# Kernel optimization log

Hardware: AMD Instinct MI355X
Metric: run time of the kernel (lower is better)

## Reference

```python
import jax, jax.numpy as jnp
import numpy as np

N_FILLERS = 10000
N_ROLES = 256
FILLER_DIM = 256
ROLE_DIM = 256
HIDDEN = 1024
B, S = 64, 128


def setup_inputs() -> dict:
    key = jax.random.key(0)
    k1, k2, k3, k4, k5, k6 = jax.random.split(key, 6)
    roles = jax.random.randint(k1, (B, S), 0, N_ROLES, dtype=jnp.int64 if jax.config.jax_enable_x64 else jnp.int32)
    hidden = jax.random.normal(k2, (1, B, HIDDEN), dtype=jnp.float32)
    filler_emb = jax.random.normal(k3, (N_FILLERS, FILLER_DIM), dtype=jnp.float32)
    role_emb = jax.random.normal(k4, (N_ROLES, ROLE_DIM), dtype=jnp.float32)
    role_emb = role_emb.at[0].set(0.0)  # padding_idx=0
    W = jax.random.normal(k5, (FILLER_DIM * ROLE_DIM, HIDDEN), dtype=jnp.float32) / np.sqrt(HIDDEN)
    b = jax.random.normal(k6, (FILLER_DIM * ROLE_DIM,), dtype=jnp.float32) * 0.01
    return {"roles": roles, "hidden": hidden, "filler_emb": filler_emb, "role_emb": role_emb, "W": W, "b": b}


def reference(roles, hidden, filler_emb, role_emb, W, b):
    fd = filler_emb.shape[1]
    rd = role_emb.shape[1]
    # input_layer: (1, B, hidden) -> (1, B, fd*rd)
    h = hidden @ W.T + b
    # transpose(0,1).transpose(1,2).view(-1, fd, rd): (B, fd, rd)
    h = jnp.transpose(h, (1, 2, 0)).reshape(-1, fd, rd)
    # role embedding with padding_idx=0 (row 0 is zero)
    role_table = role_emb.at[0].set(0.0)
    roles_e = role_table[roles]  # (B, S, rd)
    # bmm(roles_emb, hidden^T): (B, S, rd) x (B, rd, fd) -> (B, S, fd)
    fg = jnp.einsum('bsr,bfr->bsf', roles_e, h)
    # L2 distance to filler codebook via squared-norm trick: (B, S, n_fillers)
    d2 = (jnp.sum(fg * fg, axis=-1, keepdims=True)
          - 2.0 * jnp.einsum('bsf,nf->bsn', fg, filler_emb)
          + jnp.sum(filler_emb * filler_emb, axis=-1))
    dists = jnp.sqrt(jnp.maximum(d2, 0.0))
    log_probs = jax.nn.log_softmax(-dists, axis=-1)  # (B, S, n_fillers)
    preds = jnp.argmax(log_probs, axis=-1)  # top-1 indices, (B, S)
    return log_probs, preds
```

## Files before the change

### kernel.cpp

```cpp
#include <hip/hip_runtime.h>
#include <hip/hip_bf16.h>
#include <float.h>
#include <math.h>

#define ROWS 8192
#define NF   10000
#define NPAD 10240

typedef short s8v __attribute__((ext_vector_type(8)));
typedef float f4v __attribute__((ext_vector_type(4)));

#define GLD16(g, l) __builtin_amdgcn_global_load_lds((const __attribute__((address_space(1))) void*)(g), (__attribute__((address_space(3))) void*)(l), 16, 0, 0)

__device__ inline unsigned short f2bf(float x) {
  __hip_bfloat16 h = __float2bfloat16(x);
  return __builtin_bit_cast(unsigned short, h);
}
__device__ inline float bf2f(unsigned short u) {
  __hip_bfloat16 h = __builtin_bit_cast(__hip_bfloat16, u);
  return __bfloat162float(h);
}

__global__ __launch_bounds__(256) void k_cvt_filler(const float* __restrict__ filler,
                                                    unsigned short* __restrict__ fl2,
                                                    float* __restrict__ fln) {
  int row = blockIdx.x * 4 + (threadIdx.x >> 6);
  int lane = threadIdx.x & 63;
  if (row >= NPAD) return;
  if (row < NF) {
    float4 v = reinterpret_cast<const float4*>(filler + (size_t)row * 256)[lane];
    float s = v.x * v.x + v.y * v.y + v.z * v.z + v.w * v.w;
    #pragma unroll
    for (int off = 32; off >= 1; off >>= 1) s += __shfl_xor(s, off, 64);
    if (lane == 0) fln[row] = s;
    float xs[4] = {v.x, v.y, v.z, v.w};
    unsigned short h[4], lo[4];
    #pragma unroll
    for (int j = 0; j < 4; ++j) { h[j] = f2bf(xs[j]); lo[j] = f2bf(xs[j] - bf2f(h[j])); }
    uint2 hh = make_uint2(h[0] | ((unsigned)h[1] << 16), h[2] | ((unsigned)h[3] << 16));
    uint2 ll = make_uint2(lo[0] | ((unsigned)lo[1] << 16), lo[2] | ((unsigned)lo[3] << 16));
    *reinterpret_cast<uint2*>(fl2 + (size_t)row * 512 + lane * 4) = hh;
    *reinterpret_cast<uint2*>(fl2 + (size_t)row * 512 + 256 + lane * 4) = ll;
  } else {
    *reinterpret_cast<uint2*>(fl2 + (size_t)row * 512 + lane * 4) = make_uint2(0, 0);
    *reinterpret_cast<uint2*>(fl2 + (size_t)row * 512 + 256 + lane * 4) = make_uint2(0, 0);
    if (lane == 0) fln[row] = 1e30f;
  }
}

__global__ __launch_bounds__(256) void k_gemm1(const float* __restrict__ hidden,
                                               const float* __restrict__ W,
                                               const float* __restrict__ bias,
                                               float* __restrict__ ht) {
  __shared__ float As[64][68];
  __shared__ float Bs[64][136];
  __shared__ float biasS[128];
  const int tid = threadIdx.x;
  const int nbase = blockIdx.x * 128;
  const int r = nbase >> 8;
  const int f0 = nbase & 255;
  const int tm = tid >> 4, tn = tid & 15;
  const int m0 = tm * 4, n0 = tn * 8;

  if (tid < 128) biasS[tid] = bias[(size_t)(f0 + tid) * 256 + r];

  float acc[4][8];
  #pragma unroll
  for (int i = 0; i < 4; ++i)
    #pragma unroll
    for (int j = 0; j < 8; ++j) acc[i][j] = 0.f;

  for (int kt = 0; kt < 16; ++kt) {
    __syncthreads();
    #pragma unroll
    for (int i = 0; i < 4; ++i) {
      int q = tid + i * 256;
      int b = q >> 4, kq = q & 15;
      float4 v = *reinterpret_cast<const float4*>(hidden + (size_t)b * 1024 + kt * 64 + kq * 4);
      As[kq * 4 + 0][b] = v.x;
      As[kq * 4 + 1][b] = v.y;
      As[kq * 4 + 2][b] = v.z;
      As[kq * 4 + 3][b] = v.w;
    }
    #pragma unroll
    for (int i = 0; i < 8; ++i) {
      int q = tid + i * 256;
      int nl = q >> 4, kq = q & 15;
      size_t wrow = (size_t)(f0 + nl) * 256 + r;
      float4 v = *reinterpret_cast<const float4*>(W + wrow * 1024 + kt * 64 + kq * 4);
      Bs[kq * 4 + 0][nl] = v.x;
      Bs[kq * 4 + 1][nl] = v.y;
      Bs[kq * 4 + 2][nl] = v.z;
      Bs[kq * 4 + 3][nl] = v.w;
    }
    __syncthreads();
    #pragma unroll
    for (int kk = 0; kk < 64; ++kk) {
      float4 a  = *reinterpret_cast<const float4*>(&As[kk][m0]);
      float4 b0 = *reinterpret_cast<const float4*>(&Bs[kk][n0]);
      float4 b1 = *reinterpret_cast<const float4*>(&Bs[kk][n0 + 4]);
      float av[4] = {a.x, a.y, a.z, a.w};
      float bv[8] = {b0.x, b0.y, b0.z, b0.w, b1.x, b1.y, b1.z, b1.w};
      #pragma unroll
      for (int i = 0; i < 4; ++i)
        #pragma unroll
        for (int j = 0; j < 8; ++j) acc[i][j] += av[i] * bv[j];
    }
  }
  #pragma unroll
  for (int i = 0; i < 4; ++i) {
    int b = m0 + i;
    float4 o0 = make_float4(acc[i][0] + biasS[n0 + 0], acc[i][1] + biasS[n0 + 1],
                            acc[i][2] + biasS[n0 + 2], acc[i][3] + biasS[n0 + 3]);
    float4 o1 = make_float4(acc[i][4] + biasS[n0 + 4], acc[i][5] + biasS[n0 + 5],
                            acc[i][6] + biasS[n0 + 6], acc[i][7] + biasS[n0 + 7]);
    float* p = ht + (size_t)b * 65536 + nbase + n0;
    *reinterpret_cast<float4*>(p)     = o0;
    *reinterpret_cast<float4*>(p + 4) = o1;
  }
}

__global__ __launch_bounds__(256) void k_fg2(const int* __restrict__ roles,
                                             const float* __restrict__ role_emb,
                                             const float* __restrict__ ht,
                                             unsigned short* __restrict__ fg2,
                                             float* __restrict__ fgn) {
  __shared__ float As[64][40];
  __shared__ float Bs[64][264];
  __shared__ int sidx[32];
  const int tid = threadIdx.x;
  const int b = blockIdx.x >> 2;
  const int sbase = (blockIdx.x & 3) * 32;
  const int tm = tid >> 5, tn = tid & 31;
  const int m0 = tm * 4, n0 = tn * 8;
  if (tid < 32) sidx[tid] = roles[b * 128 + sbase + tid];

  float acc[4][8];
  #pragma unroll
  for (int i = 0; i < 4; ++i)
    #pragma unroll
    for (int j = 0; j < 8; ++j) acc[i][j] = 0.f;

  for (int kt = 0; kt < 4; ++kt) {
    __syncthreads();
    #pragma unroll
    for (int i = 0; i < 2; ++i) {
      int q = tid + i * 256;
      int s = q >> 4, rq = q & 15;
      float4 v = *reinterpret_cast<const float4*>(role_emb + (size_t)sidx[s] * 256 + kt * 64 + rq * 4);
      As[rq * 4 + 0][s] = v.x;
      As[rq * 4 + 1][s] = v.y;
      As[rq * 4 + 2][s] = v.z;
      As[rq * 4 + 3][s] = v.w;
    }
    #pragma unroll
    for (int i = 0; i < 16; ++i) {
      int q = tid + i * 256;
      int rr = q >> 6, fq = q & 63;
      float4 v = *reinterpret_cast<const float4*>(ht + (size_t)b * 65536 + (size_t)(kt * 64 + rr) * 256 + fq * 4);
      *reinterpret_cast<float4*>(&Bs[rr][fq * 4]) = v;
    }
    __syncthreads();
    #pragma unroll
    for (int kk = 0; kk < 64; ++kk) {
      float4 a  = *reinterpret_cast<const float4*>(&As[kk][m0]);
      float4 b0 = *reinterpret_cast<const float4*>(&Bs[kk][n0]);
      float4 b1 = *reinterpret_cast<const float4*>(&Bs[kk][n0 + 4]);
      float av[4] = {a.x, a.y, a.z, a.w};
      float bv[8] = {b0.x, b0.y, b0.z, b0.w, b1.x, b1.y, b1.z, b1.w};
      #pragma unroll
      for (int i = 0; i < 4; ++i)
        #pragma unroll
        for (int j = 0; j < 8; ++j) acc[i][j] += av[i] * bv[j];
    }
  }
  #pragma unroll
  for (int i = 0; i < 4; ++i) {
    const int grow = b * 128 + sbase + m0 + i;
    float nrm = 0.f;
    unsigned int hp[4], lp[4];
    #pragma unroll
    for (int j = 0; j < 8; j += 2) {
      float x0 = acc[i][j], x1 = acc[i][j + 1];
      nrm += x0 * x0 + x1 * x1;
      unsigned short h0 = f2bf(x0), h1 = f2bf(x1);
      unsigned short l0 = f2bf(x0 - bf2f(h0)), l1 = f2bf(x1 - bf2f(h1));
      hp[j >> 1] = h0 | ((unsigned)h1 << 16);
      lp[j >> 1] = l0 | ((unsigned)l1 << 16);
    }
    *reinterpret_cast<uint4*>(fg2 + (size_t)grow * 512 + n0)       = make_uint4(hp[0], hp[1], hp[2], hp[3]);
    *reinterpret_cast<uint4*>(fg2 + (size_t)grow * 512 + 256 + n0) = make_uint4(lp[0], lp[1], lp[2], lp[3]);
    #pragma unroll
    for (int msk = 1; msk <= 16; msk <<= 1) nrm += __shfl_xor(nrm, msk, 64);
    if (tn == 0) fgn[grow] = nrm;
  }
}

__global__ __launch_bounds__(256, 2) void k_dist(const unsigned short* __restrict__ fg2,
                                                 const unsigned short* __restrict__ fl2,
                                                 const float* __restrict__ fgn,
                                                 const float* __restrict__ fln,
                                                 float* __restrict__ out) {
  __shared__ __align__(16) char lds[2][32768];
  __shared__ float rn2s[128], cn2s[128];
  const int tid = threadIdx.x;
  const int w = tid >> 6, l = tid & 63;
  const int g = l >> 4, lr = l & 15;
  const int mt  = (blockIdx.x & 7) * 8 + ((blockIdx.x >> 3) & 7);
  const int grp = blockIdx.x >> 6;
  const int rbase = mt << 7;
  const int wm = (w >> 1) << 6, wn = (w & 1) << 6;

  if (tid < 128) rn2s[tid] = fgn[rbase + tid];

  int rowC[4], swC[4];
  #pragma unroll
  for (int t = 0; t < 4; ++t) {
    int p = tid + t * 256;
    int row = p >> 3, c = p & 7;
    rowC[t] = row;
    swC[t] = (c ^ (row & 7)) << 3;
  }
  int offA[4], offB[4];
  #pragma unroll
  for (int i = 0; i < 4; ++i) { int r = wm + i * 16 + lr; offA[i] = r * 128 + ((g ^ (r & 7)) << 4); }
  #pragma unroll
  for (int j = 0; j < 4; ++j) { int r = wn + j * 16 + lr; offB[j] = 16384 + r * 128 + ((g ^ (r & 7)) << 4); }

  auto kAof = [](int kt) { return ((kt & 3) << 6) + ((kt >= 4 && kt < 8) ? 256 : 0); };
  auto kBof = [](int kt) { return ((kt & 3) << 6) + ((kt >= 8) ? 256 : 0); };

  auto stage = [&](int buf, int kt, int nb) {
    const int kA = kAof(kt), kB = kBof(kt);
    char* bA = &lds[buf][0]     + w * 1024;
    char* bB = &lds[buf][16384] + w * 1024;
    #pragma unroll
    for (int t = 0; t < 4; ++t) {
      GLD16(fg2 + ((size_t)(rbase + rowC[t]) * 512 + kA + swC[t]), bA + t * 4096);
      GLD16(fl2 + ((size_t)(nb    + rowC[t]) * 512 + kB + swC[t]), bB + t * 4096);
    }
  };

  stage(0, 0, grp << 7);

  for (int s = 0; s < 10; ++s) {
    const int nt = grp + s * 8;
    const int nbase = nt << 7;
    if (tid < 128) cn2s[tid] = fln[nbase + tid];
    __syncthreads();
    float cnr[4];
    #pragma unroll
    for (int j = 0; j < 4; ++j) cnr[j] = cn2s[wn + j * 16 + lr];
    float rnr[4][4];
    #pragma unroll
    for (int i = 0; i < 4; ++i)
      #pragma unroll
      for (int r = 0; r < 4; ++r) rnr[i][r] = rn2s[wm + i * 16 + g * 4 + r];

    f4v acc[4][4];
    #pragma unroll
    for (int i = 0; i < 4; ++i)
      #pragma unroll
      for (int j = 0; j < 4; ++j) acc[i][j] = (f4v)0.f;

    for (int kt = 0; kt < 12; ++kt) {
      if (kt < 11)      stage((kt + 1) & 1, kt + 1, nbase);
      else if (s < 9)   stage(0, 0, (nt + 8) << 7);
      const char* A = lds[kt & 1];
      #pragma unroll
      for (int s2 = 0; s2 < 2; ++s2) {
        s8v va[4], vb[4];
        #pragma unroll
        for (int i = 0; i < 4; ++i) va[i] = *reinterpret_cast<const s8v*>(A + (offA[i] ^ (s2 << 6)));
        #pragma unroll
        for (int j = 0; j < 4; ++j) vb[j] = *reinterpret_cast<const s8v*>(A + (offB[j] ^ (s2 << 6)));
        #pragma unroll
        for (int i = 0; i < 4; ++i)
          #pragma unroll
          for (int j = 0; j < 4; ++j)
            acc[i][j] = __builtin_amdgcn_mfma_f32_16x16x32_bf16(va[i], vb[j], acc[i][j], 0, 0, 0);
      }
      __syncthreads();
    }

    float* scr = reinterpret_cast<float*>(&lds[1][0]);
    const int rem = NF - nbase;
    const int c4lim = (rem >= 128) ? 32 : (rem > 0 ? (rem >> 2) : 0);
    const int lbase = (wm >> 6) << 4;

    #pragma unroll
    for (int i = 0; i < 4; ++i) {
      #pragma unroll
      for (int j = 0; j < 4; ++j) {
        const int cloc = wn + (j << 4) + lr;
        #pragma unroll
        for (int r = 0; r < 4; ++r) {
          const int lrow = lbase + (g << 2) + r;
          float d = sqrtf(fmaxf(rnr[i][r] - 2.0f * acc[i][j][r] + cnr[j], 0.f));
          scr[lrow * 132 + cloc] = d;
        }
      }
      __syncthreads();
      #pragma unroll
      for (int t2 = 0; t2 < 4; ++t2) {
        const int id2 = tid + (t2 << 8);
        const int rr2 = id2 >> 5, c4 = id2 & 31;
        f4v v = *reinterpret_cast<const f4v*>(scr + rr2 * 132 + (c4 << 2));
        if (c4 < c4lim) {
          const int grow = rbase + ((rr2 < 16) ? ((i << 4) + rr2) : (64 + (i << 4) + rr2 - 16));
          *reinterpret_cast<f4v*>(out + (size_t)grow * NF + nbase + (c4 << 2)) = v;
        }
      }
      __syncthreads();
    }
  }
}

__global__ __launch_bounds__(256) void k_final(float* __restrict__ out) {
  const int row = blockIdx.x;
  __shared__ __align__(16) float rowd[10000];
  __shared__ float red[16];
  const int t = threadIdx.x;
  const int w = t >> 6, l = t & 63;
  float* po = out + (size_t)row * NF;

  float bd = FLT_MAX; int bi = 0;
  for (int c = t; c < 2500; c += 256) {
    f4v v = __builtin_nontemporal_load(reinterpret_cast<const f4v*>(po) + c);
    *reinterpret_cast<f4v*>(&rowd[c * 4]) = v;
    const int base = c * 4;
    if (v[0] < bd) { bd = v[0]; bi = base; }
    if (v[1] < bd) { bd = v[1]; bi = base + 1; }
    if (v[2] < bd) { bd = v[2]; bi = base + 2; }
    if (v[3] < bd) { bd = v[3]; bi = base + 3; }
  }
  #pragma unroll
  for (int msk = 1; msk <= 32; msk <<= 1) {
    float od = __shfl_xor(bd, msk, 64);
    int   oi = __shfl_xor(bi, msk, 64);
    if (od < bd || (od == bd && oi < bi)) { bd = od; bi = oi; }
  }
  if (l == 0) { red[w * 2] = bd; red[w * 2 + 1] = (float)bi; }
  __syncthreads();
  if (t == 0) {
    float m = red[0], mi = red[1];
    #pragma unroll
    for (int c = 1; c < 4; ++c) {
      float od = red[c * 2], oi = red[c * 2 + 1];
      if (od < m || (od == m && oi < mi)) { m = od; mi = oi; }
    }
    red[8] = m; red[9] = mi;
  }
  __syncthreads();
  const float m = red[8];

  float s = 0.f;
  for (int c = t; c < 2500; c += 256) {
    f4v v = *reinterpret_cast<const f4v*>(&rowd[c * 4]);
    s += __expf(m - v[0]) + __expf(m - v[1]) + __expf(m - v[2]) + __expf(m - v[3]);
  }
  #pragma unroll
  for (int msk = 1; msk <= 32; msk <<= 1) s += __shfl_xor(s, msk, 64);
  if (l == 0) red[10 + w] = s;
  __syncthreads();
  if (t == 0) {
    float S = red[10] + red[11] + red[12] + red[13];
    red[14] = logf(S) - m;
    out[(size_t)ROWS * NF + row] = red[9];
  }
  __syncthreads();
  const float L = red[14];

  for (int c = t; c < 2500; c += 256) {
    f4v v = *reinterpret_cast<const f4v*>(&rowd[c * 4]);
    v = -v - L;
    __builtin_nontemporal_store(v, reinterpret_cast<f4v*>(po) + c);
  }
}

extern "C" void kernel_launch(void* const* d_in, const int* in_sizes, int n_in,
                              void* d_out, int out_size, void* d_ws, size_t ws_size,
                              hipStream_t stream) {
  const int*   roles   = (const int*)d_in[0];
  const float* hidden  = (const float*)d_in[1];
  const float* filler  = (const float*)d_in[2];
  const float* roleemb = (const float*)d_in[3];
  const float* W       = (const float*)d_in[4];
  const float* bias    = (const float*)d_in[5];
  float* out = (float*)d_out;

  float* ws = (float*)d_ws;
  float*          ht    = ws;
  unsigned short* fg2   = (unsigned short*)(ws + 4194304);
  unsigned short* fl2   = (unsigned short*)(ws + 6291456);
  float*          fgn   = ws + 8912896;
  float*          fln   = fgn + 8192;

  k_cvt_filler<<<2560, 256, 0, stream>>>(filler, fl2, fln);
  k_gemm1<<<512, 256, 0, stream>>>(hidden, W, bias, ht);
  k_fg2<<<256, 256, 0, stream>>>(roles, roleemb, ht, fg2, fgn);
  k_dist<<<512, 256, 0, stream>>>(fg2, fl2, fgn, fln, out);
  k_final<<<8192, 256, 0, stream>>>(out);
}
```

Before: 570.9 us.

## Deepen k_dist LDS prefetch to distance two with manual waitcnt barriers

Restructures the k_dist main loop to prefetch K tiles two steps ahead, replacing __syncthreads with explicit vmcnt/lgkmcnt waits and raw s_barrier calls. All LDS fragments for a tile are loaded before the next stage is issued, and the MFMA block runs at raised wave priority. Column norms are read straight from global memory instead of going through shared memory, row norms are hoisted out of the loop, and output stores become nontemporal. The aim is to hide global-to-LDS latency and cut barrier overhead, at the cost of fragile hand-tuned waitcnt counts and a redundant stage issued on the last iteration.

```diff
diff --git a/kernel.cpp b/kernel.cpp
--- a/kernel.cpp
+++ b/kernel.cpp
@@ -202,7 +202,7 @@
                                                  const float* __restrict__ fln,
                                                  float* __restrict__ out) {
   __shared__ __align__(16) char lds[2][32768];
-  __shared__ float rn2s[128], cn2s[128];
+  __shared__ float rn2s[128];
   const int tid = threadIdx.x;
   const int w = tid >> 6, l = tid & 63;
   const int g = l >> 4, lr = l & 15;
@@ -242,45 +242,54 @@
   };
 
   stage(0, 0, grp << 7);
+  __syncthreads();
+
+  float rnr[4][4];
+  #pragma unroll
+  for (int i = 0; i < 4; ++i)
+    #pragma unroll
+    for (int r = 0; r < 4; ++r) rnr[i][r] = rn2s[wm + i * 16 + g * 4 + r];
 
   for (int s = 0; s < 10; ++s) {
     const int nt = grp + s * 8;
     const int nbase = nt << 7;
-    if (tid < 128) cn2s[tid] = fln[nbase + tid];
-    __syncthreads();
     float cnr[4];
     #pragma unroll
-    for (int j = 0; j < 4; ++j) cnr[j] = cn2s[wn + j * 16 + lr];
-    float rnr[4][4];
+    for (int j = 0; j < 4; ++j) cnr[j] = fln[nbase + wn + j * 16 + lr];
+    stage(1, 1, nbase);
+
+    f4v acc[4][4];
     #pragma unroll
     for (int i = 0; i < 4; ++i)
       #pragma unroll
-      for (int r = 0; r < 4; ++r) rnr[i][r] = rn2s[wm + i * 16 + g * 4 + r];
-
-    f4v acc[4][4];
-    #pragma unroll
-    for (int i = 0; i < 4; ++i)
-      #pragma unroll
       for (int j = 0; j < 4; ++j) acc[i][j] = (f4v)0.f;
 
     for (int kt = 0; kt < 12; ++kt) {
-      if (kt < 11)      stage((kt + 1) & 1, kt + 1, nbase);
-      else if (s < 9)   stage(0, 0, (nt + 8) << 7);
+      asm volatile("s_waitcnt vmcnt(8)" ::: "memory");
+      __builtin_amdgcn_s_barrier();
       const char* A = lds[kt & 1];
+      s8v va[2][4], vb[2][4];
       #pragma unroll
       for (int s2 = 0; s2 < 2; ++s2) {
-        s8v va[4], vb[4];
-        #pragma unroll
-        for (int i = 0; i < 4; ++i) va[i] = *reinterpret_cast<const s8v*>(A + (offA[i] ^ (s2 << 6)));
-        #pragma unroll
-        for (int j = 0; j < 4; ++j) vb[j] = *reinterpret_cast<const s8v*>(A + (offB[j] ^ (s2 << 6)));
+        #pragma unroll
+        for (int i = 0; i < 4; ++i) va[s2][i] = *reinterpret_cast<const s8v*>(A + (offA[i] ^ (s2 << 6)));
+        #pragma unroll
+        for (int j = 0; j < 4; ++j) vb[s2][j] = *reinterpret_cast<const s8v*>(A + (offB[j] ^ (s2 << 6)));
+      }
+      asm volatile("s_waitcnt lgkmcnt(0)" ::: "memory");
+      __builtin_amdgcn_sched_barrier(0);
+      __builtin_amdgcn_s_barrier();
+      if (kt < 10)       stage(kt & 1, kt + 2, nbase);
+      else if (kt == 10) stage(0, 0, (s < 9) ? ((nt + 8) << 7) : nbase);
+      __builtin_amdgcn_s_setprio(1);
+      #pragma unroll
+      for (int s2 = 0; s2 < 2; ++s2)
         #pragma unroll
         for (int i = 0; i < 4; ++i)
           #pragma unroll
           for (int j = 0; j < 4; ++j)
-            acc[i][j] = __builtin_amdgcn_mfma_f32_16x16x32_bf16(va[i], vb[j], acc[i][j], 0, 0, 0);
-      }
-      __syncthreads();
+            acc[i][j] = __builtin_amdgcn_mfma_f32_16x16x32_bf16(va[s2][i], vb[s2][j], acc[i][j], 0, 0, 0);
+      __builtin_amdgcn_s_setprio(0);
     }
 
     float* scr = reinterpret_cast<float*>(&lds[1][0]);
@@ -300,7 +309,8 @@
           scr[lrow * 132 + cloc] = d;
         }
       }
-      __syncthreads();
+      asm volatile("s_waitcnt lgkmcnt(0)" ::: "memory");
+      __builtin_amdgcn_s_barrier();
       #pragma unroll
       for (int t2 = 0; t2 < 4; ++t2) {
         const int id2 = tid + (t2 << 8);
@@ -308,10 +318,11 @@
         f4v v = *reinterpret_cast<const f4v*>(scr + rr2 * 132 + (c4 << 2));
         if (c4 < c4lim) {
           const int grow = rbase + ((rr2 < 16) ? ((i << 4) + rr2) : (64 + (i << 4) + rr2 - 16));
-          *reinterpret_cast<f4v*>(out + (size_t)grow * NF + nbase + (c4 << 2)) = v;
+          __builtin_nontemporal_store(v, reinterpret_cast<f4v*>(out + (size_t)grow * NF + nbase + (c4 << 2)));
         }
       }
-      __syncthreads();
+      asm volatile("s_waitcnt lgkmcnt(0)" ::: "memory");
+      __builtin_amdgcn_s_barrier();
     }
   }
 }
```

Result: slower. 602.7 us (+5.6%).
